# Kernel optimization log

Measured on AMD Instinct MI355X. Metric: run time of the kernel, lower is better.

## Reference

```python
import jax, jax.numpy as jnp
import numpy as np

N = 1048576        # number of time samples (rays)
V = 32             # num_videos
D = 32             # embedding_dim
F = 6              # num_frequencies
K = 2 * F + 1      # basis size: [1, sin(2^j*pi*t), cos(2^j*pi*t)]


def setup_inputs() -> dict:
    key = jax.random.key(0)
    k1, k2, k3 = jax.random.split(key, 3)
    times = jax.random.uniform(k1, (N, 1), dtype=jnp.float32)
    video_ids = jax.random.randint(k2, (N, 1), 0, V, dtype=jnp.int32)
    weights = jax.random.normal(k3, (V, D, K), dtype=jnp.float32)
    return {"times": times, "video_ids": video_ids, "weights": weights}


def _fourier_basis(t):
    # t: [N] -> [N, K] with basis [1, sin(2^j pi t), cos(2^j pi t)] j=0..F-1
    freqs = (2.0 ** jnp.arange(F, dtype=t.dtype)) * jnp.pi  # [F]
    ang = t[:, None] * freqs                                # [N, F]
    return jnp.concatenate(
        [jnp.ones_like(t)[:, None], jnp.sin(ang), jnp.cos(ang)], axis=-1
    )


def reference(times, video_ids, weights):
    shp = times.shape
    t = times.reshape(-1)                       # [N]
    vid = video_ids.reshape(-1).astype(jnp.int32)  # [N]
    basis = _fourier_basis(t)                   # [N, K]
    w = weights[vid]                            # gather: [N, D, K]
    emb = jnp.einsum('ndk,nk->nd', w, basis)    # [N, D]
    return emb.reshape((*shp[:-1], -1))
```

## Files before the change

### kernel.cpp

```cpp
#include <hip/hip_runtime.h>
#include <hip/hip_fp16.h>

#define NRAYS 1048576
#define NV 32
#define ND 32
#define NF 6
#define NK 13

typedef _Float16 h2 __attribute__((ext_vector_type(2)));
typedef float f4 __attribute__((ext_vector_type(4)));

__device__ __forceinline__ float fdot2acc(h2 a, h2 b, float c) {
#if __has_builtin(__builtin_amdgcn_fdot2)
    return __builtin_amdgcn_fdot2(a, b, c, false);
#else
    return c + (float)a.x * (float)b.x + (float)a.y * (float)b.y;
#endif
}

__device__ __forceinline__ h2 pack2(float a, float b) {
#if __has_builtin(__builtin_amdgcn_cvt_pkrtz)
    return __builtin_bit_cast(h2, __builtin_amdgcn_cvt_pkrtz(a, b));
#else
    h2 r; r.x = (_Float16)a; r.y = (_Float16)b; return r;
#endif
}

__device__ __forceinline__ float hwsin(float rev) {
#if __has_builtin(__builtin_amdgcn_sinf)
    return __builtin_amdgcn_sinf(rev);
#else
    return __sinf(6.28318530717958647692f * rev);
#endif
}
__device__ __forceinline__ float hwcos(float rev) {
#if __has_builtin(__builtin_amdgcn_cosf)
    return __builtin_amdgcn_cosf(rev);
#else
    return __cosf(6.28318530717958647692f * rev);
#endif
}

__global__ void pack_weights_kernel(const float* __restrict__ weights,
                                    unsigned* __restrict__ wpack)
{
    int j = blockIdx.x * 256 + threadIdx.x;
    if (j >= NV * 7 * 32) return;
    int v = j / 224;
    int r = j - v * 224;
    int i = r >> 5;
    int c = r & 31;
    int pos = c >> 2;
    int e = c & 3;
    int q = pos ^ (v & 7);
    int d = 4 * q + e;
    float w0 = weights[v * (ND * NK) + d * NK + 2 * i];
    float w1 = (2 * i + 1 < NK) ? weights[v * (ND * NK) + d * NK + 2 * i + 1] : 0.f;
    h2 p = pack2(w0, w1);
    wpack[j] = __builtin_bit_cast(unsigned, p);
}

__global__ __launch_bounds__(256, 5) void VideoEmbedding_kernel(
    const float* __restrict__ times,
    const int* __restrict__ vids,
    const unsigned* __restrict__ wpack,
    float* __restrict__ out)
{
    __shared__ _Float16 wl[NV * 7 * ND * 2];

    const int tid = threadIdx.x;

    {
        const uint4* src = reinterpret_cast<const uint4*>(wpack);
        uint4* dst = reinterpret_cast<uint4*>(wl);
#pragma unroll
        for (int j = 0; j < 7; ++j)
            dst[tid + j * 256] = src[tid + j * 256];
    }
    __syncthreads();

    const int q = tid & 7;
    const int nslots = (gridDim.x * 256) >> 3;
    int ray = ((blockIdx.x * 256) + tid) >> 3;

    int rA = ray < NRAYS ? ray : 0;
    int rB = ray + nslots < NRAYS ? ray + nslots : 0;
    float tA = times[rA], tB = times[rB];
    int vA = vids[rA], vB = vids[rB];

    while (ray < NRAYS) {
        const int ray2 = ray + 2 * nslots;
        const int rC = ray2 < NRAYS ? ray2 : 0;
        const float tC = times[rC];
        const int vC = vids[rC];

        float sv[NF], cv[NF];
        sv[0] = hwsin(0.5f * tA);
        cv[0] = hwcos(0.5f * tA);
#pragma unroll
        for (int j = 1; j < NF; ++j) {
            float sj = sv[j - 1], cj = cv[j - 1];
            sv[j] = 2.f * sj * cj;
            cv[j] = fmaf(-2.f * sj, sj, 1.f);
        }

        h2 bp[7];
        bp[0] = pack2(1.0f, sv[0]);
        bp[1] = pack2(sv[1], sv[2]);
        bp[2] = pack2(sv[3], sv[4]);
        bp[3] = pack2(sv[5], cv[0]);
        bp[4] = pack2(cv[1], cv[2]);
        bp[5] = pack2(cv[3], cv[4]);
        bp[6] = pack2(cv[5], 0.0f);

        const unsigned pos = (unsigned)(q ^ (vA & 7));
        const unsigned base = (unsigned)vA * 448u + pos * 8u;
        uint4 w[7];
#pragma unroll
        for (int i = 0; i < 7; ++i)
            w[i] = *reinterpret_cast<const uint4*>(&wl[base + i * 64]);

        float a0 = 0.f, a1 = 0.f, a2 = 0.f, a3 = 0.f;
#pragma unroll
        for (int i = 0; i < 7; ++i) {
            a0 = fdot2acc(__builtin_bit_cast(h2, w[i].x), bp[i], a0);
            a1 = fdot2acc(__builtin_bit_cast(h2, w[i].y), bp[i], a1);
            a2 = fdot2acc(__builtin_bit_cast(h2, w[i].z), bp[i], a2);
            a3 = fdot2acc(__builtin_bit_cast(h2, w[i].w), bp[i], a3);
        }

        f4 res;
        res.x = a0; res.y = a1; res.z = a2; res.w = a3;
        reinterpret_cast<f4*>(out)[(size_t)ray * 8 + q] = res;

        ray += nslots;
        tA = tB; vA = vB;
        tB = tC; vB = vC;
    }
}

extern "C" void kernel_launch(void* const* d_in, const int* in_sizes, int n_in,
                              void* d_out, int out_size, void* d_ws, size_t ws_size,
                              hipStream_t stream) {
    const float* times = (const float*)d_in[0];
    const int* vids = (const int*)d_in[1];
    const float* weights = (const float*)d_in[2];
    float* out = (float*)d_out;
    unsigned* wpack = (unsigned*)d_ws;

    hipLaunchKernelGGL(pack_weights_kernel, dim3(28), dim3(256), 0, stream,
                       weights, wpack);
    hipLaunchKernelGGL(VideoEmbedding_kernel, dim3(1280), dim3(256), 0, stream,
                       times, vids, wpack, out);
}
```

Measured before the change: 36.65 us.

## Sort rays by video id within each 256-ray chunk before LDS weight lookup

Each block now processes 256-ray chunks and counting-sorts them by video id in shared memory (histogram, warp prefix scan, atomic scatter). Rays sharing a video then land in the same wavefront, which cuts LDS bank conflicts and divergence on the weight reads. Outputs are scattered back to their original positions with nontemporal stores. The cost is several __syncthreads per chunk, shared-memory atomics, and losing the previous software prefetch of times and ids.

```diff
diff --git a/kernel.cpp b/kernel.cpp
--- a/kernel.cpp
+++ b/kernel.cpp
@@ -67,6 +67,9 @@
     float* __restrict__ out)
 {
     __shared__ _Float16 wl[NV * 7 * ND * 2];
+    __shared__ int hist[NV];
+    __shared__ float s_t[256];
+    __shared__ int s_meta[256];
 
     const int tid = threadIdx.x;
 
@@ -77,65 +80,83 @@
         for (int j = 0; j < 7; ++j)
             dst[tid + j * 256] = src[tid + j * 256];
     }
-    __syncthreads();
 
     const int q = tid & 7;
-    const int nslots = (gridDim.x * 256) >> 3;
-    int ray = ((blockIdx.x * 256) + tid) >> 3;
+    const int g = tid >> 3;
 
-    int rA = ray < NRAYS ? ray : 0;
-    int rB = ray + nslots < NRAYS ? ray + nslots : 0;
-    float tA = times[rA], tB = times[rB];
-    int vA = vids[rA], vB = vids[rB];
+    const int NCHUNK = NRAYS / 256;
+    for (int chunk = blockIdx.x; chunk < NCHUNK; chunk += gridDim.x) {
+        const int base = chunk * 256;
+        const float t = times[base + tid];
+        const int vid = vids[base + tid];
 
-    while (ray < NRAYS) {
-        const int ray2 = ray + 2 * nslots;
-        const int rC = ray2 < NRAYS ? ray2 : 0;
-        const float tC = times[rC];
-        const int vC = vids[rC];
+        if (tid < NV) hist[tid] = 0;
+        __syncthreads();
+        atomicAdd(&hist[vid], 1);
+        __syncthreads();
+        if (tid < NV) {
+            int c = hist[tid];
+            int sum = c;
+#pragma unroll
+            for (int off = 1; off < NV; off <<= 1) {
+                int n = __shfl_up(sum, off, NV);
+                if (tid >= off) sum += n;
+            }
+            hist[tid] = sum - c;
+        }
+        __syncthreads();
+        {
+            int pos = atomicAdd(&hist[vid], 1);
+            s_t[pos] = t;
+            s_meta[pos] = (vid << 8) | tid;
+        }
+        __syncthreads();
 
-        float sv[NF], cv[NF];
-        sv[0] = hwsin(0.5f * tA);
-        cv[0] = hwcos(0.5f * tA);
+#pragma unroll 2
+        for (int p = 0; p < 8; ++p) {
+            const int slot = p * 32 + g;
+            const float ts = s_t[slot];
+            const int meta = s_meta[slot];
+            const int v = meta >> 8;
+            const int lidx = meta & 255;
+
+            float sv[NF], cv[NF];
+            sv[0] = hwsin(0.5f * ts);
+            cv[0] = hwcos(0.5f * ts);
 #pragma unroll
-        for (int j = 1; j < NF; ++j) {
-            float sj = sv[j - 1], cj = cv[j - 1];
-            sv[j] = 2.f * sj * cj;
-            cv[j] = fmaf(-2.f * sj, sj, 1.f);
+            for (int j = 1; j < NF; ++j) {
+                float sj = sv[j - 1], cj = cv[j - 1];
+                sv[j] = 2.f * sj * cj;
+                cv[j] = fmaf(-2.f * sj, sj, 1.f);
+            }
+
+            h2 bp[7];
+            bp[0] = pack2(1.0f, sv[0]);
+            bp[1] = pack2(sv[1], sv[2]);
+            bp[2] = pack2(sv[3], sv[4]);
+            bp[3] = pack2(sv[5], cv[0]);
+            bp[4] = pack2(cv[1], cv[2]);
+            bp[5] = pack2(cv[3], cv[4]);
+            bp[6] = pack2(cv[5], 0.0f);
+
+            const unsigned posq = (unsigned)(q ^ (v & 7));
+            const unsigned baddr = (unsigned)v * 448u + posq * 8u;
+            float a0 = 0.f, a1 = 0.f, a2 = 0.f, a3 = 0.f;
+#pragma unroll
+            for (int i = 0; i < 7; ++i) {
+                uint4 w = *reinterpret_cast<const uint4*>(&wl[baddr + i * 64]);
+                a0 = fdot2acc(__builtin_bit_cast(h2, w.x), bp[i], a0);
+                a1 = fdot2acc(__builtin_bit_cast(h2, w.y), bp[i], a1);
+                a2 = fdot2acc(__builtin_bit_cast(h2, w.z), bp[i], a2);
+                a3 = fdot2acc(__builtin_bit_cast(h2, w.w), bp[i], a3);
+            }
+
+            f4 res;
+            res.x = a0; res.y = a1; res.z = a2; res.w = a3;
+            __builtin_nontemporal_store(res,
+                reinterpret_cast<f4*>(out) + (size_t)(base + lidx) * 8 + q);
         }
-
-        h2 bp[7];
-        bp[0] = pack2(1.0f, sv[0]);
-        bp[1] = pack2(sv[1], sv[2]);
-        bp[2] = pack2(sv[3], sv[4]);
-        bp[3] = pack2(sv[5], cv[0]);
-        bp[4] = pack2(cv[1], cv[2]);
-        bp[5] = pack2(cv[3], cv[4]);
-        bp[6] = pack2(cv[5], 0.0f);
-
-        const unsigned pos = (unsigned)(q ^ (vA & 7));
-        const unsigned base = (unsigned)vA * 448u + pos * 8u;
-        uint4 w[7];
-#pragma unroll
-        for (int i = 0; i < 7; ++i)
-            w[i] = *reinterpret_cast<const uint4*>(&wl[base + i * 64]);
-
-        float a0 = 0.f, a1 = 0.f, a2 = 0.f, a3 = 0.f;
-#pragma unroll
-        for (int i = 0; i < 7; ++i) {
-            a0 = fdot2acc(__builtin_bit_cast(h2, w[i].x), bp[i], a0);
-            a1 = fdot2acc(__builtin_bit_cast(h2, w[i].y), bp[i], a1);
-            a2 = fdot2acc(__builtin_bit_cast(h2, w[i].z), bp[i], a2);
-            a3 = fdot2acc(__builtin_bit_cast(h2, w[i].w), bp[i], a3);
-        }
-
-        f4 res;
-        res.x = a0; res.y = a1; res.z = a2; res.w = a3;
-        reinterpret_cast<f4*>(out)[(size_t)ray * 8 + q] = res;
-
-        ray += nslots;
-        tA = tB; vA = vB;
-        tB = tC; vB = vC;
+        __syncthreads();
     }
 }
 
```

Measured after the change: 39.07 us. +6.6%, slower.

## Software-pipeline LDS weight loads and deepen global prefetch to three rays

Applied to the files above, without the earlier changes.

The main loop now double-buffers the per-ray weight vectors read from LDS, loading the next ray's weights while computing the current one. It also prefetches times and video ids three iterations ahead instead of two. The aim is to hide LDS and global load latency behind the fdot2 arithmetic. In exchange it uses more VGPRs (two 7x uint4 buffers), which may reduce occupancy under the launch bound. It also drops the initial ray<NRAYS guard and clamps prefetch indices instead of zeroing them.

```diff
diff --git a/kernel.cpp b/kernel.cpp
--- a/kernel.cpp
+++ b/kernel.cpp
@@ -41,6 +41,25 @@
 #endif
 }
 
+__device__ __forceinline__ void make_basis(float t, h2 bp[7]) {
+    float sv[NF], cv[NF];
+    sv[0] = hwsin(0.5f * t);
+    cv[0] = hwcos(0.5f * t);
+#pragma unroll
+    for (int j = 1; j < NF; ++j) {
+        float sj = sv[j - 1], cj = cv[j - 1];
+        sv[j] = 2.f * sj * cj;
+        cv[j] = fmaf(-2.f * sj, sj, 1.f);
+    }
+    bp[0] = pack2(1.0f, sv[0]);
+    bp[1] = pack2(sv[1], sv[2]);
+    bp[2] = pack2(sv[3], sv[4]);
+    bp[3] = pack2(sv[5], cv[0]);
+    bp[4] = pack2(cv[1], cv[2]);
+    bp[5] = pack2(cv[3], cv[4]);
+    bp[6] = pack2(cv[5], 0.0f);
+}
+
 __global__ void pack_weights_kernel(const float* __restrict__ weights,
                                     unsigned* __restrict__ wpack)
 {
@@ -56,8 +75,7 @@
     int d = 4 * q + e;
     float w0 = weights[v * (ND * NK) + d * NK + 2 * i];
     float w1 = (2 * i + 1 < NK) ? weights[v * (ND * NK) + d * NK + 2 * i + 1] : 0.f;
-    h2 p = pack2(w0, w1);
-    wpack[j] = __builtin_bit_cast(unsigned, p);
+    wpack[j] = __builtin_bit_cast(unsigned, pack2(w0, w1));
 }
 
 __global__ __launch_bounds__(256, 5) void VideoEmbedding_kernel(
@@ -69,7 +87,6 @@
     __shared__ _Float16 wl[NV * 7 * ND * 2];
 
     const int tid = threadIdx.x;
-
     {
         const uint4* src = reinterpret_cast<const uint4*>(wpack);
         uint4* dst = reinterpret_cast<uint4*>(wl);
@@ -80,63 +97,67 @@
     __syncthreads();
 
     const int q = tid & 7;
-    const int nslots = (gridDim.x * 256) >> 3;
+    const int gs = (gridDim.x * 256) >> 3;
     int ray = ((blockIdx.x * 256) + tid) >> 3;
 
-    int rA = ray < NRAYS ? ray : 0;
-    int rB = ray + nslots < NRAYS ? ray + nslots : 0;
-    float tA = times[rA], tB = times[rB];
-    int vA = vids[rA], vB = vids[rB];
+    float t0, t1, t2;
+    int v0, v1, v2;
+    t0 = times[ray]; v0 = vids[ray];
+    int rr = min(ray + gs, NRAYS - 1);
+    t1 = times[rr]; v1 = vids[rr];
+    rr = min(ray + 2 * gs, NRAYS - 1);
+    t2 = times[rr]; v2 = vids[rr];
 
-    while (ray < NRAYS) {
-        const int ray2 = ray + 2 * nslots;
-        const int rC = ray2 < NRAYS ? ray2 : 0;
-        const float tC = times[rC];
-        const int vC = vids[rC];
+    uint4 wA[7], wB[7];
 
-        float sv[NF], cv[NF];
-        sv[0] = hwsin(0.5f * tA);
-        cv[0] = hwcos(0.5f * tA);
-#pragma unroll
-        for (int j = 1; j < NF; ++j) {
-            float sj = sv[j - 1], cj = cv[j - 1];
-            sv[j] = 2.f * sj * cj;
-            cv[j] = fmaf(-2.f * sj, sj, 1.f);
-        }
-
-        h2 bp[7];
-        bp[0] = pack2(1.0f, sv[0]);
-        bp[1] = pack2(sv[1], sv[2]);
-        bp[2] = pack2(sv[3], sv[4]);
-        bp[3] = pack2(sv[5], cv[0]);
-        bp[4] = pack2(cv[1], cv[2]);
-        bp[5] = pack2(cv[3], cv[4]);
-        bp[6] = pack2(cv[5], 0.0f);
-
-        const unsigned pos = (unsigned)(q ^ (vA & 7));
-        const unsigned base = (unsigned)vA * 448u + pos * 8u;
-        uint4 w[7];
+    {
+        const unsigned base = (unsigned)v0 * 448u + (unsigned)(q ^ (v0 & 7)) * 8u;
 #pragma unroll
         for (int i = 0; i < 7; ++i)
-            w[i] = *reinterpret_cast<const uint4*>(&wl[base + i * 64]);
+            wA[i] = *reinterpret_cast<const uint4*>(&wl[base + i * 64]);
+    }
 
-        float a0 = 0.f, a1 = 0.f, a2 = 0.f, a3 = 0.f;
-#pragma unroll
-        for (int i = 0; i < 7; ++i) {
-            a0 = fdot2acc(__builtin_bit_cast(h2, w[i].x), bp[i], a0);
-            a1 = fdot2acc(__builtin_bit_cast(h2, w[i].y), bp[i], a1);
-            a2 = fdot2acc(__builtin_bit_cast(h2, w[i].z), bp[i], a2);
-            a3 = fdot2acc(__builtin_bit_cast(h2, w[i].w), bp[i], a3);
-        }
+#define STAGE(WCUR, WNEXT)                                                    \
+    {                                                                         \
+                                               \
+        rr = min(ray + 3 * gs, NRAYS - 1);                                    \
+        const float t3 = times[rr];                                           \
+        const int v3 = vids[rr];                                              \
+                                    \
+        {                                                                     \
+            const unsigned nb =                                               \
+                (unsigned)v1 * 448u + (unsigned)(q ^ (v1 & 7)) * 8u;          \
+            _Pragma("unroll")                                                 \
+            for (int i = 0; i < 7; ++i)                                       \
+                WNEXT[i] = *reinterpret_cast<const uint4*>(&wl[nb + i * 64]); \
+        }                                                                     \
+                                   \
+        {                                                                     \
+            h2 bp[7];                                                         \
+            make_basis(t0, bp);                                               \
+            float a0 = 0.f, a1 = 0.f, a2 = 0.f, a3 = 0.f;                     \
+            _Pragma("unroll")                                                 \
+            for (int i = 0; i < 7; ++i) {                                     \
+                a0 = fdot2acc(__builtin_bit_cast(h2, WCUR[i].x), bp[i], a0);  \
+                a1 = fdot2acc(__builtin_bit_cast(h2, WCUR[i].y), bp[i], a1);  \
+                a2 = fdot2acc(__builtin_bit_cast(h2, WCUR[i].z), bp[i], a2);  \
+                a3 = fdot2acc(__builtin_bit_cast(h2, WCUR[i].w), bp[i], a3);  \
+            }                                                                 \
+            f4 res;                                                           \
+            res.x = a0; res.y = a1; res.z = a2; res.w = a3;                   \
+            reinterpret_cast<f4*>(out)[(size_t)ray * 8 + q] = res;            \
+        }                                                                     \
+        ray += gs;                                                            \
+        if (ray >= NRAYS) break;                                              \
+        t0 = t1; t1 = t2; t2 = t3;                                            \
+        v0 = v1; v1 = v2; v2 = v3;                                            \
+    }
 
-        f4 res;
-        res.x = a0; res.y = a1; res.z = a2; res.w = a3;
-        reinterpret_cast<f4*>(out)[(size_t)ray * 8 + q] = res;
-
-        ray += nslots;
-        tA = tB; vA = vB;
-        tB = tC; vB = vC;
+    while (true) {
+        STAGE(wA, wB)
+        STAGE(wB, wA)
     }
+#undef STAGE
 }
 
 extern "C" void kernel_launch(void* const* d_in, const int* in_sizes, int n_in,
```

Measured after the change: 34.98 us. -4.6%, faster.
